# Optimization experiments

Hardware: AMD Instinct MI355X
Metric: run time of the kernel (lower is better)

Reference implementation:

```python
import jax, jax.numpy as jnp
import numpy as np
from functools import partial

# dims
BATCH, L, H = 1, 512, 2048
NH, HD = 64, 64            # num heads, head dim
INTER = NH * HD            # 4096
G, N = 4, 64               # n_groups, ssm state size
K = 4                      # conv kernel
CONV = INTER + 2 * G * N   # 4608
PROJ = INTER + CONV + NH   # z, xBC, dt
EPS = 1e-5


def rmsnorm(x, w, eps=EPS):
    xf = x.astype(jnp.float32)
    v = jnp.mean(xf * xf, axis=-1, keepdims=True)
    return (xf * jax.lax.rsqrt(v + eps)).astype(x.dtype) * w


def setup_inputs() -> dict:
    key = jax.random.key(0)
    ks = jax.random.split(key, 12)
    rn = lambda k, s, sc=1.0: sc * jax.random.normal(k, s, dtype=jnp.float32)
    return {
        "hidden_states": rn(ks[0], (BATCH, L, H)),
        "residual": rn(ks[1], (BATCH, L, H)),
        "norm_w": 1.0 + rn(ks[2], (H,), 0.02),
        "in_proj_w": rn(ks[3], (H, PROJ), 0.02),
        "conv_w": rn(ks[4], (CONV, K), 0.2),
        "conv_b": rn(ks[5], (CONV,), 0.02),
        "A_log": jnp.log(jax.random.uniform(ks[6], (NH,), minval=1.0, maxval=16.0)),
        "dt_bias": rn(ks[7], (NH,), 0.5),
        "D": rn(ks[8], (NH,), 0.5),
        "gn_w": 1.0 + rn(ks[9], (INTER,), 0.02),
        "out_proj_w": rn(ks[10], (INTER, H), 0.02),
    }


def reference(hidden_states, residual, norm_w, in_proj_w, conv_w, conv_b,
              A_log, dt_bias, D, gn_w, out_proj_w):
    B_ = hidden_states.shape[0]
    # fused add + RMSNorm (residual is not None path)
    x = hidden_states + residual
    new_residual = x
    hs = rmsnorm(x, norm_w)

    # in_proj: [B,L,H] -> [B,L,PROJ] split into z | xBC | dt
    proj = jnp.einsum('blh,hp->blp', hs, in_proj_w)
    z = proj[..., :INTER]
    xBC = proj[..., INTER:INTER + CONV]
    dt = proj[..., INTER + CONV:]

    # causal depthwise conv of width K, then SiLU
    xp = jnp.pad(xBC, ((0, 0), (K - 1, 0), (0, 0)))
    conv = sum(xp[:, k:k + L, :] * conv_w[None, None, :, k] for k in range(K))
    xBC = jax.nn.silu(conv + conv_b)

    xh = xBC[..., :INTER].reshape(B_, L, NH, HD)
    Bm = xBC[..., INTER:INTER + G * N].reshape(B_, L, G, N)
    Cm = xBC[..., INTER + G * N:].reshape(B_, L, G, N)

    dt = jax.nn.softplus(dt + dt_bias)          # [B,L,NH]
    A = -jnp.exp(A_log)                         # [NH]
    dA = jnp.exp(dt * A)                        # [B,L,NH]

    hpg = NH // G
    Bh = jnp.repeat(Bm, hpg, axis=2)            # [B,L,NH,N]
    Ch = jnp.repeat(Cm, hpg, axis=2)

    def step(h, inp):
        dA_t, dt_t, x_t, B_t, C_t = inp
        # h: [B,NH,HD,N]
        h = h * dA_t[:, :, None, None] + (dt_t[:, :, None] * x_t)[..., None] * B_t[:, :, None, :]
        y = jnp.einsum('bhdn,bhn->bhd', h, C_t)
        return h, y

    h0 = jnp.zeros((B_, NH, HD, N), dtype=jnp.float32)
    xs = (jnp.moveaxis(dA, 1, 0), jnp.moveaxis(dt, 1, 0), jnp.moveaxis(xh, 1, 0),
          jnp.moveaxis(Bh, 1, 0), jnp.moveaxis(Ch, 1, 0))
    _, ys = jax.lax.scan(step, h0, xs)          # [L,B,NH,HD]
    y = jnp.moveaxis(ys, 0, 1) + xh * D[None, None, :, None]
    y = y.reshape(B_, L, INTER)

    # gated RMSNorm then out_proj
    y = rmsnorm(y * jax.nn.silu(z), gn_w)
    out = jnp.einsum('bli,ih->blh', y, out_proj_w)
    return out, new_residual
```

## Files before the change

### kernel.cpp

```cpp
#include <hip/hip_runtime.h>
#include <stdint.h>

#define LSEQ 512
#define HDIM 2048
#define NH 64
#define HD 64
#define INTER 4096
#define NG 4
#define NSTATE 64
#define CONVC 4608
#define PROJC 8768
#define EPS 1e-5f
#define CL 64
#define NC 8
#define NHDN (NH * HD * NSTATE)

typedef __attribute__((ext_vector_type(8))) short bf16x8;
typedef __attribute__((ext_vector_type(4))) short short4v;
typedef __attribute__((ext_vector_type(4))) float f32x4;

__device__ __forceinline__ short f2bf(float f) {
  union { float f; uint32_t u; } v; v.f = f;
  uint32_t r = v.u + 0x7FFFu + ((v.u >> 16) & 1u);
  return (short)(r >> 16);
}

__device__ __forceinline__ float bf2f(short s) {
  union { uint32_t u; float f; } v; v.u = ((uint32_t)(uint16_t)s) << 16;
  return v.f;
}

__device__ __forceinline__ float siluf(float v) {
  return v / (1.f + expf(-v));
}

__device__ __forceinline__ int xcd_swizzle(int orig, int nwg) {
  int q = nwg >> 3, r = nwg & 7;
  int xcd = orig & 7, idx = orig >> 3;
  return (xcd < r ? xcd * (q + 1) : r * (q + 1) + (xcd - r) * q) + idx;
}

__global__ __launch_bounds__(256) void k_add_rmsnorm(
    const float* __restrict__ hid, const float* __restrict__ res,
    const float* __restrict__ w, float* __restrict__ resid_out,
    short* __restrict__ hsb) {
  __shared__ float sred[4];
  const int row = blockIdx.x, tid = threadIdx.x;
  const float4* h4 = (const float4*)(hid + (size_t)row * HDIM);
  const float4* r4 = (const float4*)(res + (size_t)row * HDIM);
  float4* ro4 = (float4*)(resid_out + (size_t)row * HDIM);
  float4 a0 = h4[tid], b0 = r4[tid];
  float4 a1 = h4[tid + 256], b1 = r4[tid + 256];
  float4 xa, xb;
  xa.x = a0.x + b0.x; xa.y = a0.y + b0.y; xa.z = a0.z + b0.z; xa.w = a0.w + b0.w;
  xb.x = a1.x + b1.x; xb.y = a1.y + b1.y; xb.z = a1.z + b1.z; xb.w = a1.w + b1.w;
  ro4[tid] = xa; ro4[tid + 256] = xb;
  float ss = xa.x*xa.x + xa.y*xa.y + xa.z*xa.z + xa.w*xa.w
           + xb.x*xb.x + xb.y*xb.y + xb.z*xb.z + xb.w*xb.w;
  #pragma unroll
  for (int off = 32; off >= 1; off >>= 1) ss += __shfl_down(ss, off);
  if ((tid & 63) == 0) sred[tid >> 6] = ss;
  __syncthreads();
  float tot = sred[0] + sred[1] + sred[2] + sred[3];
  float rs = rsqrtf(tot / (float)HDIM + EPS);
  int e0 = tid * 4, e1 = (tid + 256) * 4;
  short4v s0, s1;
  s0.x = f2bf(xa.x * rs * w[e0+0]); s0.y = f2bf(xa.y * rs * w[e0+1]);
  s0.z = f2bf(xa.z * rs * w[e0+2]); s0.w = f2bf(xa.w * rs * w[e0+3]);
  s1.x = f2bf(xb.x * rs * w[e1+0]); s1.y = f2bf(xb.y * rs * w[e1+1]);
  s1.z = f2bf(xb.z * rs * w[e1+2]); s1.w = f2bf(xb.w * rs * w[e1+3]);
  *(short4v*)(hsb + (size_t)row * HDIM + e0) = s0;
  *(short4v*)(hsb + (size_t)row * HDIM + e1) = s1;
}

template <int BM, int KS>
__global__ __launch_bounds__(256) void k_gemm_fB(
    const short* __restrict__ A, const float* __restrict__ Bw,
    float* __restrict__ C, int M, int N, int K) {
  __shared__ short lA[2][BM * 64];
  __shared__ short lB[2][64 * 64];
  const int tid = threadIdx.x, lane = tid & 63, wid = tid >> 6;
  constexpr int MR = BM / 32;
  constexpr int WROWS = BM / 2;

  const int NMB = M / BM, NNB = N / 64;
  const int nwg = NMB * NNB * KS;
  int wg = xcd_swizzle(blockIdx.x, nwg);
  const int mi = wg % NMB;
  int rest = wg / NMB;
  const int zi = (KS > 1) ? (rest % KS) : 0;
  const int ni = (KS > 1) ? (rest / KS) : rest;
  const int m0 = mi * BM, n0 = ni * 64;
  const int wm = wid >> 1, wn = wid & 1;

  const int lrow8 = lane >> 3;
  const int cswz = ((lane & 7) ^ lrow8) * 8;

  const int Kc = K / KS, kbase = zi * Kc;
  float* Cp = C + (size_t)zi * M * N;

  auto stageA = [&](int buf, int kt) {
    #pragma unroll
    for (int r2 = 0; r2 < MR; ++r2) {
      int idx = r2 * 4 + wid;
      __builtin_amdgcn_global_load_lds(
          (const __attribute__((address_space(1))) int*)(A + (size_t)(m0 + idx * 8 + lrow8) * K + kt + cswz),
          (__attribute__((address_space(3))) int*)(&lA[buf][idx * 512]),
          16, 0, 0);
    }
  };

  float breg[16];
  auto loadB = [&](int kt) {
    #pragma unroll
    for (int r = 0; r < 2; ++r)
      #pragma unroll
      for (int j = 0; j < 8; ++j)
        breg[r * 8 + j] = Bw[(size_t)(kt + wid * 16 + r * 8 + j) * N + n0 + lane];
  };
  auto writeB = [&](int buf) {
    #pragma unroll
    for (int r = 0; r < 2; ++r) {
      bf16x8 v;
      #pragma unroll
      for (int j = 0; j < 8; ++j) v[j] = f2bf(breg[r * 8 + j]);
      int ko = wid * 2 + r;
      *(bf16x8*)&lB[buf][lane * 64 + ((ko ^ (lane & 7)) << 3)] = v;
    }
  };

  f32x4 acc[MR][2] = {};
  const int lrow = lane & 15, lkb = (lane >> 4) * 8;
  const int NT = Kc >> 6;
  loadB(kbase);
  stageA(0, kbase);
  writeB(0);
  asm volatile("s_waitcnt vmcnt(0)" ::: "memory");
  __builtin_amdgcn_s_barrier();
  for (int t = 0; t < NT; ++t) {
    int cur = t & 1;
    if (t + 1 < NT) {
      loadB(kbase + (t + 1) * 64);
      stageA(cur ^ 1, kbase + (t + 1) * 64);
    }
    #pragma unroll
    for (int kk = 0; kk < 2; ++kk) {
      bf16x8 a[MR], b[2];
      #pragma unroll
      for (int m = 0; m < MR; ++m) {
        int row = wm * WROWS + m * 16 + lrow;
        int colel = (kk * 32 + lkb) ^ ((row & 7) << 3);
        a[m] = *(const bf16x8*)&lA[cur][row * 64 + colel];
      }
      #pragma unroll
      for (int n = 0; n < 2; ++n) {
        int row = wn * 32 + n * 16 + lrow;
        int colel = (kk * 32 + lkb) ^ ((row & 7) << 3);
        b[n] = *(const bf16x8*)&lB[cur][row * 64 + colel];
      }
      #pragma unroll
      for (int m = 0; m < MR; ++m)
        #pragma unroll
        for (int n = 0; n < 2; ++n)
          acc[m][n] = __builtin_amdgcn_mfma_f32_16x16x32_bf16(a[m], b[n], acc[m][n], 0, 0, 0);
    }
    if (t + 1 < NT) writeB(cur ^ 1);
    asm volatile("s_waitcnt vmcnt(0)" ::: "memory");
    __builtin_amdgcn_s_barrier();
  }
  #pragma unroll
  for (int m = 0; m < MR; ++m) {
    int row = m0 + wm * WROWS + m * 16 + (lane >> 4) * 4;
    int col = n0 + wn * 32 + (lane & 15);
    #pragma unroll
    for (int n = 0; n < 2; ++n)
      #pragma unroll
      for (int r = 0; r < 4; ++r)
        Cp[(size_t)(row + r) * N + col + n * 16] = acc[m][n][r];
  }
}

__global__ __launch_bounds__(256) void k_reduce2(
    const float* __restrict__ p, float* __restrict__ out, int n) {
  int i = (blockIdx.x * 256 + threadIdx.x) * 4;
  float4 a = *(const float4*)(p + i);
  float4 b = *(const float4*)(p + n + i);
  float4 o;
  o.x = a.x + b.x; o.y = a.y + b.y; o.z = a.z + b.z; o.w = a.w + b.w;
  *(float4*)(out + i) = o;
}

__global__ __launch_bounds__(256) void k_conv(
    const float* __restrict__ proj, const float* __restrict__ cw,
    const float* __restrict__ cb, float* __restrict__ convo) {
  const int c = blockIdx.x * 256 + threadIdx.x;
  const int l0 = blockIdx.y * 64;
  const float w0 = cw[c*4+0], w1 = cw[c*4+1], w2 = cw[c*4+2], w3 = cw[c*4+3];
  const float bias = cb[c];
  float x0 = 0.f, x1 = 0.f, x2 = 0.f;
  if (l0 > 0) {
    x0 = proj[(size_t)(l0-3) * PROJC + INTER + c];
    x1 = proj[(size_t)(l0-2) * PROJC + INTER + c];
    x2 = proj[(size_t)(l0-1) * PROJC + INTER + c];
  }
  for (int l = l0; l < l0 + 64; ++l) {
    float x3 = proj[(size_t)l * PROJC + INTER + c];
    float accv = bias + x0*w0 + x1*w1 + x2*w2 + x3*w3;
    convo[(size_t)l * CONVC + c] = siluf(accv);
    x0 = x1; x1 = x2; x2 = x3;
  }
}

__global__ __launch_bounds__(256) void k_dt(
    const float* __restrict__ proj, const float* __restrict__ A_log,
    const float* __restrict__ dt_bias, float* __restrict__ dtb,
    float* __restrict__ ldab) {
  const int l = blockIdx.x * 4 + (threadIdx.x >> 6);
  const int h = threadIdx.x & 63;
  float v = proj[(size_t)l * PROJC + INTER + CONVC + h] + dt_bias[h];
  float dt = v > 20.f ? v : log1pf(expf(v));
  float lda = dt * (-expf(A_log[h]));
  dtb[h * LSEQ + l] = dt;
  ldab[h * LSEQ + l] = lda;
}

__global__ __launch_bounds__(256) void k_ssd(
    const float* __restrict__ convo, const float* __restrict__ dtb,
    const float* __restrict__ ldab, const float* __restrict__ Dp,
    float* __restrict__ ybuf, float* __restrict__ hend,
    float* __restrict__ Pbuf, float* __restrict__ cdbuf) {
  __shared__ __align__(16) short Xt[64 * 72];
  __shared__ __align__(16) short Bs[64 * 72];
  __shared__ __align__(16) short Cs[64 * 72];
  __shared__ __align__(16) short Btw[64 * 72];
  __shared__ __align__(16) short Ms[64 * 72];
  __shared__ float s_s[64], s_dt[64], s_w[64];
  const int c = blockIdx.x, head = blockIdx.y;
  const int g = head >> 4;
  const int tid = threadIdx.x, lane = tid & 63, wid = tid >> 6;
  const int l0 = c * CL;
  const float* xbase = convo + (size_t)l0 * CONVC + head * HD;
  const float* Bbase = convo + (size_t)l0 * CONVC + INTER + g * NSTATE;
  const float* Cbase = convo + (size_t)l0 * CONVC + INTER + NG * NSTATE + g * NSTATE;

  if (tid < 64) {
    float ps = ldab[head * LSEQ + l0 + tid];
    #pragma unroll
    for (int o = 1; o < 64; o <<= 1) {
      float u = __shfl_up(ps, o);
      if (tid >= o) ps += u;
    }
    float dtv = dtb[head * LSEQ + l0 + tid];
    s_s[tid] = ps;
    s_dt[tid] = dtv;
    float s63 = __shfl(ps, 63);
    s_w[tid] = __expf(s63 - ps) * dtv;
    cdbuf[head * LSEQ + l0 + tid] = __expf(ps);
    if (tid == 63) Pbuf[c * NH + head] = __expf(ps);
  }
  #pragma unroll
  for (int rep = 0; rep < 4; ++rep) {
    int l = (tid >> 4) + rep * 16;
    int d = (tid & 15) * 4;
    size_t roff = (size_t)l * CONVC;
    float4 xv = *(const float4*)(xbase + roff + d);
    Xt[(d + 0) * 72 + l] = f2bf(xv.x);
    Xt[(d + 1) * 72 + l] = f2bf(xv.y);
    Xt[(d + 2) * 72 + l] = f2bf(xv.z);
    Xt[(d + 3) * 72 + l] = f2bf(xv.w);
    float4 bv = *(const float4*)(Bbase + roff + d);
    short4v b4; b4.x = f2bf(bv.x); b4.y = f2bf(bv.y); b4.z = f2bf(bv.z); b4.w = f2bf(bv.w);
    *(short4v*)&Bs[l * 72 + d] = b4;
    float4 cv = *(const float4*)(Cbase + roff + d);
    short4v c4; c4.x = f2bf(cv.x); c4.y = f2bf(cv.y); c4.z = f2bf(cv.z); c4.w = f2bf(cv.w);
    *(short4v*)&Cs[l * 72 + d] = c4;
  }
  __syncthreads();
  #pragma unroll
  for (int rep = 0; rep < 16; ++rep) {
    int idx = rep * 256 + tid;
    int l = idx >> 6, n = idx & 63;
    Btw[n * 72 + l] = f2bf(bf2f(Bs[l * 72 + n]) * s_w[l]);
  }
  __syncthreads();
  const int lrow = lane & 15, lkb = (lane >> 4) * 8;
  f32x4 sacc[4] = {};
  f32x4 hacc[4] = {};
  #pragma unroll
  for (int kk = 0; kk < 2; ++kk) {
    bf16x8 ac = *(const bf16x8*)&Cs[(wid * 16 + lrow) * 72 + kk * 32 + lkb];
    bf16x8 ax = *(const bf16x8*)&Xt[(wid * 16 + lrow) * 72 + kk * 32 + lkb];
    #pragma unroll
    for (int t4 = 0; t4 < 4; ++t4) {
      bf16x8 bb = *(const bf16x8*)&Bs[(t4 * 16 + lrow) * 72 + kk * 32 + lkb];
      bf16x8 bw = *(const bf16x8*)&Btw[(t4 * 16 + lrow) * 72 + kk * 32 + lkb];
      sacc[t4] = __builtin_amdgcn_mfma_f32_16x16x32_bf16(ac, bb, sacc[t4], 0, 0, 0);
      hacc[t4] = __builtin_amdgcn_mfma_f32_16x16x32_bf16(ax, bw, hacc[t4], 0, 0, 0);
    }
  }
  float* hb = hend + ((size_t)c * NH + head) * (HD * NSTATE);
  #pragma unroll
  for (int t4 = 0; t4 < 4; ++t4) {
    int j = t4 * 16 + lrow;
    float sj = s_s[j], dtj = s_dt[j];
    #pragma unroll
    for (int r = 0; r < 4; ++r) {
      int i = wid * 16 + (lane >> 4) * 4 + r;
      float m = (j <= i) ? __expf(s_s[i] - sj) * dtj * sacc[t4][r] : 0.f;
      Ms[i * 72 + j] = f2bf(m);
      hb[i * NSTATE + j] = hacc[t4][r];
    }
  }
  __syncthreads();
  f32x4 yacc[4] = {};
  #pragma unroll
  for (int kk = 0; kk < 2; ++kk) {
    bf16x8 am = *(const bf16x8*)&Ms[(wid * 16 + lrow) * 72 + kk * 32 + lkb];
    #pragma unroll
    for (int t4 = 0; t4 < 4; ++t4) {
      bf16x8 bx = *(const bf16x8*)&Xt[(t4 * 16 + lrow) * 72 + kk * 32 + lkb];
      yacc[t4] = __builtin_amdgcn_mfma_f32_16x16x32_bf16(am, bx, yacc[t4], 0, 0, 0);
    }
  }
  const float Dv = Dp[head];
  #pragma unroll
  for (int t4 = 0; t4 < 4; ++t4) {
    int d = t4 * 16 + lrow;
    #pragma unroll
    for (int r = 0; r < 4; ++r) {
      int i = wid * 16 + (lane >> 4) * 4 + r;
      float xv = bf2f(Xt[d * 72 + i]);
      ybuf[(size_t)(l0 + i) * INTER + head * HD + d] = yacc[t4][r] + xv * Dv;
    }
  }
}

__global__ __launch_bounds__(256) void k_scan_combine(
    const float* __restrict__ hend, const float* __restrict__ Pbuf,
    float* __restrict__ hinbuf) {
  const int e = blockIdx.x * 256 + threadIdx.x;
  const int head = e >> 12;
  float h = 0.f;
  #pragma unroll
  for (int c = 1; c < NC; ++c) {
    h = Pbuf[(c - 1) * NH + head] * h + hend[(size_t)(c - 1) * NHDN + e];
    hinbuf[(size_t)c * NHDN + e] = h;
  }
}

__global__ __launch_bounds__(256) void k_scan_fixup(
    const float* __restrict__ convo, const float* __restrict__ hinbuf,
    const float* __restrict__ cdbuf, float* __restrict__ ybuf) {
  __shared__ float sh[NSTATE][HD + 1];
  __shared__ float sc[CL][NSTATE];
  __shared__ float scd[CL];
  const int bid = blockIdx.x;
  const int c = (bid >> 6) + 1, head = bid & 63, g = head >> 4;
  const int t = threadIdx.x;
  #pragma unroll
  for (int i = 0; i < 16; ++i) {
    int idx = t + i * 256;
    int d = idx >> 6, n = idx & 63;
    sh[n][d] = hinbuf[(size_t)c * NHDN + head * (HD * NSTATE) + idx];
  }
  #pragma unroll
  for (int i = 0; i < 16; ++i) {
    int idx = t + i * 256;
    int ll = idx >> 6, n = idx & 63;
    sc[ll][n] = convo[(size_t)(c * CL + ll) * CONVC + INTER + NG * NSTATE + g * NSTATE + n];
  }
  if (t < CL) scd[t] = cdbuf[head * LSEQ + c * CL + t];
  __syncthreads();
  const int d = t & 63, w = t >> 6;
  #pragma unroll
  for (int i = 0; i < 4; ++i) {
    int l0 = i * 16 + w * 4;
    float a0 = 0.f, a1 = 0.f, a2 = 0.f, a3 = 0.f;
    for (int n = 0; n < NSTATE; ++n) {
      float hv = sh[n][d];
      a0 += hv * sc[l0 + 0][n];
      a1 += hv * sc[l0 + 1][n];
      a2 += hv * sc[l0 + 2][n];
      a3 += hv * sc[l0 + 3][n];
    }
    size_t base = (size_t)(c * CL + l0) * INTER + head * HD + d;
    ybuf[base + 0 * INTER] += scd[l0 + 0] * a0;
    ybuf[base + 1 * INTER] += scd[l0 + 1] * a1;
    ybuf[base + 2 * INTER] += scd[l0 + 2] * a2;
    ybuf[base + 3 * INTER] += scd[l0 + 3] * a3;
  }
}

__global__ __launch_bounds__(256) void k_gated_norm(
    const float* __restrict__ ybuf, const float* __restrict__ proj,
    const float* __restrict__ gw, short* __restrict__ y2b) {
  __shared__ float sred[4];
  const int row = blockIdx.x, tid = threadIdx.x;
  const float4* y4 = (const float4*)(ybuf + (size_t)row * INTER);
  const float4* z4 = (const float4*)(proj + (size_t)row * PROJC);
  float g[16];
  float ss = 0.f;
  #pragma unroll
  for (int i = 0; i < 4; ++i) {
    float4 y = y4[tid + i * 256];
    float4 z = z4[tid + i * 256];
    float g0 = y.x * siluf(z.x), g1 = y.y * siluf(z.y);
    float g2 = y.z * siluf(z.z), g3 = y.w * siluf(z.w);
    g[i*4+0] = g0; g[i*4+1] = g1; g[i*4+2] = g2; g[i*4+3] = g3;
    ss += g0*g0 + g1*g1 + g2*g2 + g3*g3;
  }
  #pragma unroll
  for (int off = 32; off >= 1; off >>= 1) ss += __shfl_down(ss, off);
  if ((tid & 63) == 0) sred[tid >> 6] = ss;
  __syncthreads();
  float tot = sred[0] + sred[1] + sred[2] + sred[3];
  float rs = rsqrtf(tot / (float)INTER + EPS);
  #pragma unroll
  for (int i = 0; i < 4; ++i) {
    int e = (tid + i * 256) * 4;
    short4v s;
    s.x = f2bf(g[i*4+0] * rs * gw[e+0]);
    s.y = f2bf(g[i*4+1] * rs * gw[e+1]);
    s.z = f2bf(g[i*4+2] * rs * gw[e+2]);
    s.w = f2bf(g[i*4+3] * rs * gw[e+3]);
    *(short4v*)(y2b + (size_t)row * INTER + e) = s;
  }
}

extern "C" void kernel_launch(void* const* d_in, const int* in_sizes, int n_in,
                              void* d_out, int out_size, void* d_ws, size_t ws_size,
                              hipStream_t stream) {
  const float* hid     = (const float*)d_in[0];
  const float* res     = (const float*)d_in[1];
  const float* norm_w  = (const float*)d_in[2];
  const float* w1      = (const float*)d_in[3];
  const float* cw      = (const float*)d_in[4];
  const float* cb      = (const float*)d_in[5];
  const float* A_log   = (const float*)d_in[6];
  const float* dt_bias = (const float*)d_in[7];
  const float* Dp      = (const float*)d_in[8];
  const float* gw      = (const float*)d_in[9];
  const float* w2      = (const float*)d_in[10];

  float* out = (float*)d_out;
  float* resid_out = out + (size_t)LSEQ * HDIM;

  char* ws = (char*)d_ws;
  short* hsb  = (short*)(ws);
  float* hend   = (float*)(ws + 2097152);
  float* p2     = (float*)(ws + 2097152);
  float* hinbuf = (float*)(ws + 10485760);
  float* Pbuf   = (float*)(ws + 18874368);
  float* cdbuf  = (float*)(ws + 18876416);
  float* proj = (float*)(ws + 38010880);
  float* convo= (float*)(ws + 55967744);
  float* dtb  = (float*)(ws + 65404928);
  float* ldab = (float*)(ws + 65536000);
  float* ybuf = (float*)(ws + 65667072);
  short* y2b  = (short*)(ws + 74055680);

  k_add_rmsnorm<<<LSEQ, 256, 0, stream>>>(hid, res, norm_w, resid_out, hsb);
  k_gemm_fB<128, 1><<<(LSEQ/128)*(PROJC/64), 256, 0, stream>>>(hsb, w1, proj, LSEQ, PROJC, HDIM);
  k_conv<<<dim3(CONVC/256, NC), 256, 0, stream>>>(proj, cw, cb, convo);
  k_dt<<<LSEQ/4, 256, 0, stream>>>(proj, A_log, dt_bias, dtb, ldab);
  k_ssd<<<dim3(NC, NH), 256, 0, stream>>>(convo, dtb, ldab, Dp, ybuf, hend, Pbuf, cdbuf);
  k_scan_combine<<<NHDN/256, 256, 0, stream>>>(hend, Pbuf, hinbuf);
  k_scan_fixup<<<(NC-1)*NH, 256, 0, stream>>>(convo, hinbuf, cdbuf, ybuf);
  k_gated_norm<<<LSEQ, 256, 0, stream>>>(ybuf, proj, gw, y2b);
  k_gemm_fB<64, 2><<<(LSEQ/64)*(HDIM/64)*2, 256, 0, stream>>>(y2b, w2, p2, LSEQ, HDIM, INTER);
  k_reduce2<<<LSEQ*HDIM/1024, 256, 0, stream>>>(p2, out, LSEQ*HDIM);
}
```

Before: 150.4 us.

## Deepen GEMM pipeline to two tiles in flight with triple-buffered A

Restructures the fp32-weight GEMM main loop so two K-tiles of loads are in flight at once. A is triple-buffered in LDS and B goes through two register buffers, with precise vmcnt waits in place of full drains, unrolled by two with sched_barriers. The goal is to hide global-load latency behind MFMA work instead of waiting for all loads every iteration. It costs more LDS and registers, which may lower occupancy. It also assumes NT is even and at least 2, and relies on hand-counted vmcnt values.

```diff
diff --git a/kernel.cpp b/kernel.cpp
--- a/kernel.cpp
+++ b/kernel.cpp
@@ -77,7 +77,7 @@
 __global__ __launch_bounds__(256) void k_gemm_fB(
     const short* __restrict__ A, const float* __restrict__ Bw,
     float* __restrict__ C, int M, int N, int K) {
-  __shared__ short lA[2][BM * 64];
+  __shared__ short lA[3][BM * 64];
   __shared__ short lB[2][64 * 64];
   const int tid = threadIdx.x, lane = tid & 63, wid = tid >> 6;
   constexpr int MR = BM / 32;
@@ -110,20 +110,20 @@
     }
   };
 
-  float breg[16];
-  auto loadB = [&](int kt) {
+  float breg0[16], breg1[16];
+  auto loadB = [&](int kt, float (&br)[16]) {
     #pragma unroll
     for (int r = 0; r < 2; ++r)
       #pragma unroll
       for (int j = 0; j < 8; ++j)
-        breg[r * 8 + j] = Bw[(size_t)(kt + wid * 16 + r * 8 + j) * N + n0 + lane];
+        br[r * 8 + j] = Bw[(size_t)(kt + wid * 16 + r * 8 + j) * N + n0 + lane];
   };
-  auto writeB = [&](int buf) {
+  auto writeB = [&](int buf, float (&br)[16]) {
     #pragma unroll
     for (int r = 0; r < 2; ++r) {
       bf16x8 v;
       #pragma unroll
-      for (int j = 0; j < 8; ++j) v[j] = f2bf(breg[r * 8 + j]);
+      for (int j = 0; j < 8; ++j) v[j] = f2bf(br[r * 8 + j]);
       int ko = wid * 2 + r;
       *(bf16x8*)&lB[buf][lane * 64 + ((ko ^ (lane & 7)) << 3)] = v;
     }
@@ -131,18 +131,8 @@
 
   f32x4 acc[MR][2] = {};
   const int lrow = lane & 15, lkb = (lane >> 4) * 8;
-  const int NT = Kc >> 6;
-  loadB(kbase);
-  stageA(0, kbase);
-  writeB(0);
-  asm volatile("s_waitcnt vmcnt(0)" ::: "memory");
-  __builtin_amdgcn_s_barrier();
-  for (int t = 0; t < NT; ++t) {
-    int cur = t & 1;
-    if (t + 1 < NT) {
-      loadB(kbase + (t + 1) * 64);
-      stageA(cur ^ 1, kbase + (t + 1) * 64);
-    }
+
+  auto compute = [&](int a3, int b2) {
     #pragma unroll
     for (int kk = 0; kk < 2; ++kk) {
       bf16x8 a[MR], b[2];
@@ -150,13 +140,13 @@
       for (int m = 0; m < MR; ++m) {
         int row = wm * WROWS + m * 16 + lrow;
         int colel = (kk * 32 + lkb) ^ ((row & 7) << 3);
-        a[m] = *(const bf16x8*)&lA[cur][row * 64 + colel];
+        a[m] = *(const bf16x8*)&lA[a3][row * 64 + colel];
       }
       #pragma unroll
       for (int n = 0; n < 2; ++n) {
         int row = wn * 32 + n * 16 + lrow;
         int colel = (kk * 32 + lkb) ^ ((row & 7) << 3);
-        b[n] = *(const bf16x8*)&lB[cur][row * 64 + colel];
+        b[n] = *(const bf16x8*)&lB[b2][row * 64 + colel];
       }
       #pragma unroll
       for (int m = 0; m < MR; ++m)
@@ -164,10 +154,62 @@
         for (int n = 0; n < 2; ++n)
           acc[m][n] = __builtin_amdgcn_mfma_f32_16x16x32_bf16(a[m], b[n], acc[m][n], 0, 0, 0);
     }
-    if (t + 1 < NT) writeB(cur ^ 1);
-    asm volatile("s_waitcnt vmcnt(0)" ::: "memory");
+  };
+
+  const int NT = Kc >> 6;
+
+  loadB(kbase, breg0);
+  stageA(0, kbase);
+  loadB(kbase + 64, breg1);
+  stageA(1, kbase + 64);
+  if constexpr (MR == 4) asm volatile("s_waitcnt vmcnt(24)" ::: "memory");
+  else                   asm volatile("s_waitcnt vmcnt(22)" ::: "memory");
+  writeB(0, breg0);
+  if constexpr (MR == 4) asm volatile("s_waitcnt vmcnt(20)" ::: "memory");
+  else                   asm volatile("s_waitcnt vmcnt(18)" ::: "memory");
+  asm volatile("s_waitcnt lgkmcnt(0)" ::: "memory");
+  __builtin_amdgcn_s_barrier();
+  __builtin_amdgcn_sched_barrier(0);
+
+  for (int t = 0; t + 3 < NT; t += 2) {
+    loadB(kbase + (t + 2) * 64, breg0);
+    stageA((t + 2) % 3, kbase + (t + 2) * 64);
+    __builtin_amdgcn_sched_barrier(0);
+    compute(t % 3, 0);
+    __builtin_amdgcn_sched_barrier(0);
+    if constexpr (MR == 4) asm volatile("s_waitcnt vmcnt(24)" ::: "memory");
+    else                   asm volatile("s_waitcnt vmcnt(22)" ::: "memory");
+    writeB(1, breg1);
+    if constexpr (MR == 4) asm volatile("s_waitcnt vmcnt(20)" ::: "memory");
+    else                   asm volatile("s_waitcnt vmcnt(18)" ::: "memory");
+    asm volatile("s_waitcnt lgkmcnt(0)" ::: "memory");
     __builtin_amdgcn_s_barrier();
-  }
+    __builtin_amdgcn_sched_barrier(0);
+    loadB(kbase + (t + 3) * 64, breg1);
+    stageA((t + 3) % 3, kbase + (t + 3) * 64);
+    __builtin_amdgcn_sched_barrier(0);
+    compute((t + 1) % 3, 1);
+    __builtin_amdgcn_sched_barrier(0);
+    if constexpr (MR == 4) asm volatile("s_waitcnt vmcnt(24)" ::: "memory");
+    else                   asm volatile("s_waitcnt vmcnt(22)" ::: "memory");
+    writeB(0, breg0);
+    if constexpr (MR == 4) asm volatile("s_waitcnt vmcnt(20)" ::: "memory");
+    else                   asm volatile("s_waitcnt vmcnt(18)" ::: "memory");
+    asm volatile("s_waitcnt lgkmcnt(0)" ::: "memory");
+    __builtin_amdgcn_s_barrier();
+    __builtin_amdgcn_sched_barrier(0);
+  }
+  compute((NT - 2) % 3, 0);
+  __builtin_amdgcn_sched_barrier(0);
+  if constexpr (MR == 4) asm volatile("s_waitcnt vmcnt(4)" ::: "memory");
+  else                   asm volatile("s_waitcnt vmcnt(2)" ::: "memory");
+  writeB(1, breg1);
+  asm volatile("s_waitcnt vmcnt(0)" ::: "memory");
+  asm volatile("s_waitcnt lgkmcnt(0)" ::: "memory");
+  __builtin_amdgcn_s_barrier();
+  __builtin_amdgcn_sched_barrier(0);
+  compute((NT - 1) % 3, 1);
+
   #pragma unroll
   for (int m = 0; m < MR; ++m) {
     int row = m0 + wm * WROWS + m * 16 + (lane >> 4) * 4;
```

Measured after the change: 166.8 us. +10.9%, slower.
